# Kernel tuning notes

Hardware: AMD Instinct MI355X
Metric: run time of the kernel (lower is better)

The kernel has to match this reference:

```python
import jax, jax.numpy as jnp
import numpy as np

B, T, C = 128, 512, 1024  # batch, time (fixed by `line` buffer), channels


def fft_convolve(a, b):
    """Linear convolution via zero-padded FFT, sliced to a's length.
    a: (1, C, T) kernel, b: (B, C, T) signal. Returns (B, C, T)."""
    n = a.shape[-1]
    a_pad = jnp.pad(a, ((0, 0), (0, 0), (0, n)))
    b_pad = jnp.pad(b, ((0, 0), (0, 0), (0, n)))
    spec = jnp.fft.rfft(a_pad, axis=-1) * jnp.fft.rfft(b_pad, axis=-1)
    return jnp.fft.irfft(spec, n=2 * n, axis=-1)[..., :n]


def setup_inputs() -> dict:
    key = jax.random.key(0)
    k1, k2, k3, k4, k5 = jax.random.split(key, 5)
    bound = 1.0 / np.sqrt(C)  # nn.Linear default init range
    x = jax.random.normal(k1, (B, T, C), dtype=jnp.float32)
    W_proj = jax.random.uniform(k2, (C, C), jnp.float32, -bound, bound)
    W_values = jax.random.uniform(k3, (C, C), jnp.float32, -bound, bound)
    gain = jax.random.uniform(k4, (1, 1, C), jnp.float32, 0.01, 1.0)
    pow_ = jax.random.uniform(k5, (1, C, 1), jnp.float32, -6.0, 6.0)
    line = jnp.linspace(1.0, 0.0, T, dtype=jnp.float32)[None, None, :]  # (1,1,T)
    return {"x": x, "W_proj": W_proj, "W_values": W_values,
            "gain": gain, "pow_": pow_, "line": line}


def reference(x, W_proj, W_values, gain, pow_, line):
    # proj and values (bias-free Linears)
    h = jnp.einsum('btc,dc->btd', x, W_proj)          # (B,T,C)
    v = jnp.einsum('btc,dc->btd', h, W_values)        # (B,T,C)
    # learned power-law kernel, one decay per channel: (1,C,T)
    z = line ** (2.0 + jax.nn.sigmoid(pow_) * 100.0)
    # FFT long convolution along time
    y = fft_convolve(z, jnp.transpose(v, (0, 2, 1)))  # (B,C,T)
    y = jnp.transpose(y, (0, 2, 1))                    # (B,T,C)
    return jax.nn.relu(y * gain)
```

## Files before the change

### kernel.cpp

```cpp
#include <hip/hip_runtime.h>
#include <hip/hip_bf16.h>

#define B_ 128
#define T_ 512
#define C_ 1024

typedef __attribute__((ext_vector_type(8))) short short8;
typedef __attribute__((ext_vector_type(4))) float f32x4;

__device__ __forceinline__ unsigned short f2bf(float f){
  unsigned u; __builtin_memcpy(&u, &f, 4);
  u += 0x7FFFu + ((u >> 16) & 1u);
  return (unsigned short)(u >> 16);
}

typedef __attribute__((address_space(3))) unsigned lds_u32_t;
typedef __attribute__((address_space(1))) unsigned glb_u32_t;
__device__ __forceinline__ void gload16(const void* g, void* l){
  __builtin_amdgcn_global_load_lds((const glb_u32_t*)g, (lds_u32_t*)l, 16, 0, 0);
}

__global__ void cast_f32_bf16(const float* __restrict__ in, unsigned short* __restrict__ out, long n){
  long i = (long)blockIdx.x * blockDim.x + threadIdx.x;
  long stride = (long)gridDim.x * blockDim.x;
  for (long j = i * 4; j < n; j += stride * 4){
    float4 v = *(const float4*)(in + j);
    ushort4 o; o.x = f2bf(v.x); o.y = f2bf(v.y); o.z = f2bf(v.z); o.w = f2bf(v.w);
    *(ushort4*)(out + j) = o;
  }
}

__global__ void transpose_cast(const float* __restrict__ in, unsigned short* __restrict__ out){
  __shared__ float tile[32][33];
  int c0 = blockIdx.x * 32, e0 = blockIdx.y * 32;
  int tx = threadIdx.x, ty = threadIdx.y;
  for (int r = 0; r < 32; r += 8)
    tile[ty + r][tx] = in[(size_t)(e0 + ty + r) * C_ + c0 + tx];
  __syncthreads();
  for (int r = 0; r < 32; r += 8)
    out[(size_t)(c0 + ty + r) * C_ + e0 + tx] = f2bf(tile[tx][ty + r]);
}

__global__ __launch_bounds__(256) void gemm_bt_bf16(
    const unsigned short* __restrict__ A,
    const unsigned short* __restrict__ Bt,
    unsigned short* __restrict__ Cc,
    int M, int N, int K)
{
  __shared__ short As[128 * 32];
  __shared__ short Bs[128 * 32];
  const int tid  = threadIdx.x;
  const int lane = tid & 63;
  const int wave = tid >> 6;
  const int wr = wave >> 1, wc = wave & 1;
  const int lr = lane & 15, kg = lane >> 4;
  const int m0 = blockIdx.x * 128;
  const int n0 = blockIdx.y * 128;

  f32x4 acc[4][4];
  #pragma unroll
  for (int mi = 0; mi < 4; mi++)
    #pragma unroll
    for (int ni = 0; ni < 4; ni++)
      acc[mi][ni] = (f32x4){0.f, 0.f, 0.f, 0.f};

  const int r1 = tid >> 2, ch1 = tid & 3;
  char* abase = (char*)As + (tid & ~63) * 16;
  char* bbase = (char*)Bs + (tid & ~63) * 16;

  for (int k0 = 0; k0 < K; k0 += 32){
    __syncthreads();
    gload16(A  + (size_t)(m0 + r1)      * K + k0 + ch1 * 8, abase);
    gload16(A  + (size_t)(m0 + 64 + r1) * K + k0 + ch1 * 8, abase + 4096);
    gload16(Bt + (size_t)(n0 + r1)      * K + k0 + ch1 * 8, bbase);
    gload16(Bt + (size_t)(n0 + 64 + r1) * K + k0 + ch1 * 8, bbase + 4096);
    __syncthreads();

    short8 af[4], bfr[4];
    #pragma unroll
    for (int mi = 0; mi < 4; mi++)
      af[mi] = *(const short8*)&As[(wr * 64 + mi * 16 + lr) * 32 + kg * 8];
    #pragma unroll
    for (int ni = 0; ni < 4; ni++)
      bfr[ni] = *(const short8*)&Bs[(wc * 64 + ni * 16 + lr) * 32 + kg * 8];
    #pragma unroll
    for (int mi = 0; mi < 4; mi++)
      #pragma unroll
      for (int ni = 0; ni < 4; ni++)
        acc[mi][ni] = __builtin_amdgcn_mfma_f32_16x16x32_bf16(af[mi], bfr[ni], acc[mi][ni], 0, 0, 0);
  }

  #pragma unroll
  for (int mi = 0; mi < 4; mi++)
    #pragma unroll
    for (int ni = 0; ni < 4; ni++){
      int n = n0 + wc * 64 + ni * 16 + lr;
      int mb = m0 + wr * 64 + mi * 16 + kg * 4;
      #pragma unroll
      for (int j = 0; j < 4; j++)
        Cc[(size_t)(mb + j) * N + n] = f2bf(acc[mi][ni][j]);
    }
}

#define SWZ(x) ((x) ^ ((((x) >> 7) & 3) << 4))

#define STAGE_A(kt, kh) { \
  int d_ = wv * 1024 + ln * 16; int o_ = SWZ(d_); \
  gload16(Ag + (size_t)(m0 + (o_ >> 6)) * 1024 + (kt) * 64 + (kh) * 32 + ((o_ >> 4) & 3) * 8, \
          ldsc + ((kt) & 1) * 32768 + (kh) * 16384 + wv * 1024); \
  d_ += 8192; o_ = SWZ(d_); \
  gload16(Ag + (size_t)(m0 + (o_ >> 6)) * 1024 + (kt) * 64 + (kh) * 32 + ((o_ >> 4) & 3) * 8, \
          ldsc + ((kt) & 1) * 32768 + (kh) * 16384 + 8192 + wv * 1024); }

#define STAGE_B(kt, kh) { \
  int d_ = wv * 1024 + ln * 16; int o_ = SWZ(d_); \
  gload16(Bg + (size_t)(n0 + (o_ >> 6)) * 1024 + (kt) * 64 + (kh) * 32 + ((o_ >> 4) & 3) * 8, \
          ldsc + 65536 + ((kt) & 1) * 32768 + (kh) * 16384 + wv * 1024); \
  d_ += 8192; o_ = SWZ(d_); \
  gload16(Bg + (size_t)(n0 + (o_ >> 6)) * 1024 + (kt) * 64 + (kh) * 32 + ((o_ >> 4) & 3) * 8, \
          ldsc + 65536 + ((kt) & 1) * 32768 + (kh) * 16384 + 8192 + wv * 1024); }

__global__ __launch_bounds__(512, 2) void gemm256_vt(
    const unsigned short* __restrict__ Ag,
    const unsigned short* __restrict__ Bg,
    unsigned short* __restrict__ vt)
{
  extern __shared__ char ldsc[];
  typedef __attribute__((address_space(3))) char lds_char;
  lds_char* lds3 = (lds_char*)ldsc;
  const int tid = threadIdx.x;
  const int ln  = tid & 63;
  const int wv  = tid >> 6;
  const int wr  = wv >> 2;
  const int wc  = wv & 3;
  const int lr  = ln & 15, kg = ln >> 4;
  const int m0  = blockIdx.y * 256;
  const int n0  = blockIdx.x * 256;

  f32x4 acc[8][4];
  #pragma unroll
  for (int mi = 0; mi < 8; mi++)
    #pragma unroll
    for (int ni = 0; ni < 4; ni++)
      acc[mi][ni] = (f32x4){0.f, 0.f, 0.f, 0.f};

  STAGE_A(0, 0); STAGE_A(0, 1); STAGE_B(0, 0); STAGE_B(0, 1);

  short8 af[2][8], bf2[2][4];

  #pragma unroll 1
  for (int t = 0; t < 16; ++t){
    const int S = t & 1;
    if (t < 15){
      STAGE_A(t + 1, 0); STAGE_A(t + 1, 1); STAGE_B(t + 1, 0); STAGE_B(t + 1, 1);
      __builtin_amdgcn_sched_barrier(0);
      asm volatile("s_waitcnt vmcnt(8)");
      __builtin_amdgcn_sched_barrier(0);
    } else {
      __builtin_amdgcn_sched_barrier(0);
      asm volatile("s_waitcnt vmcnt(0)");
      __builtin_amdgcn_sched_barrier(0);
    }
    __builtin_amdgcn_s_barrier();
    __builtin_amdgcn_sched_barrier(0);

    #pragma unroll
    for (int kk = 0; kk < 2; ++kk){
      #pragma unroll
      for (int mi = 0; mi < 8; mi++){
        int off = S * 32768 + kk * 16384 + (wr * 128 + mi * 16 + lr) * 64 + kg * 16;
        unsigned a_ = (unsigned)(size_t)(lds3 + SWZ(off));
        asm volatile("ds_read_b128 %0, %1" : "=v"(af[kk][mi]) : "v"(a_));
      }
      #pragma unroll
      for (int ni = 0; ni < 4; ni++){
        int off = 65536 + S * 32768 + kk * 16384 + (wc * 64 + ni * 16 + lr) * 64 + kg * 16;
        unsigned a_ = (unsigned)(size_t)(lds3 + SWZ(off));
        asm volatile("ds_read_b128 %0, %1" : "=v"(bf2[kk][ni]) : "v"(a_));
      }
    }

    asm volatile("s_waitcnt lgkmcnt(12)");
    __builtin_amdgcn_sched_barrier(0);
    __builtin_amdgcn_s_setprio(1);
    #pragma unroll
    for (int mi = 0; mi < 8; mi++)
      #pragma unroll
      for (int ni = 0; ni < 4; ni++)
        acc[mi][ni] = __builtin_amdgcn_mfma_f32_16x16x32_bf16(af[0][mi], bf2[0][ni], acc[mi][ni], 0, 0, 0);
    __builtin_amdgcn_s_setprio(0);

    asm volatile("s_waitcnt lgkmcnt(0)");
    __builtin_amdgcn_sched_barrier(0);
    __builtin_amdgcn_s_setprio(1);
    #pragma unroll
    for (int mi = 0; mi < 8; mi++)
      #pragma unroll
      for (int ni = 0; ni < 4; ni++)
        acc[mi][ni] = __builtin_amdgcn_mfma_f32_16x16x32_bf16(af[1][mi], bf2[1][ni], acc[mi][ni], 0, 0, 0);
    __builtin_amdgcn_s_setprio(0);
    __builtin_amdgcn_sched_barrier(0);
    __builtin_amdgcn_s_barrier();
  }

  #pragma unroll
  for (int mi = 0; mi < 8; mi++)
    #pragma unroll
    for (int ni = 0; ni < 4; ni++){
      int n  = n0 + wc * 64 + ni * 16 + lr;
      int mb = m0 + wr * 128 + mi * 16 + kg * 4;
      int bb = mb >> 9, t = mb & 511;
      ushort4 o;
      o.x = f2bf(acc[mi][ni][0]); o.y = f2bf(acc[mi][ni][1]);
      o.z = f2bf(acc[mi][ni][2]); o.w = f2bf(acc[mi][ni][3]);
      *(ushort4*)&vt[((size_t)n * B_ + bb) * T_ + t] = o;
    }
}

__global__ void band_prep(const float* __restrict__ pw, const float* __restrict__ line,
                          unsigned short* __restrict__ band){
  const int c = blockIdx.x, d32 = blockIdx.y;
  const float p = pw[c];
  const float e = 2.0f + 100.0f / (1.0f + expf(-p));
  const int tid = threadIdx.x;
  for (int idx = tid; idx < 1280; idx += 256){
    int i = idx / 40, j = idx - i * 40;
    int k = d32 * 32 + i - j;
    float z = 0.f;
    if (j < 32 && k >= 0 && k < T_){
      float lv = line[k];
      z = (lv > 0.f) ? expf(e * logf(lv)) : 0.f;
    }
    band[((size_t)c * 16 + d32) * 1280 + idx] = f2bf(z);
  }
}

__global__ __launch_bounds__(256) void conv_mfma(
    const unsigned short* __restrict__ vt,
    const unsigned short* __restrict__ band,
    const float* __restrict__ gain,
    unsigned short* __restrict__ Ybf)
{
  __shared__ short Bs[128 * 32];
  __shared__ short Ab[16 * 1280];
  const int c   = blockIdx.x;
  const int t0  = blockIdx.y << 7;
  const int tid = threadIdx.x, lane = tid & 63, wave = tid >> 6;
  const int wr = wave >> 1, wc = wave & 1, lr = lane & 15, kg = lane >> 4;
  const int K  = t0 + 128;
  const int nb = (t0 >> 5) + 4;

  {
    const unsigned short* src = band + (size_t)c * (16 * 1280);
    const int nch = nb * 160;
    for (int q0 = 0; q0 < nch; q0 += 256){
      int q = q0 + tid;
      char* dst = (char*)Ab + q0 * 16 + wave * 1024;
      if (q < nch) gload16(src + (size_t)q * 8, dst);
    }
  }

  f32x4 acc[4][4];
  #pragma unroll
  for (int mi = 0; mi < 4; mi++)
    #pragma unroll
    for (int ni = 0; ni < 4; ni++)
      acc[mi][ni] = (f32x4){0.f, 0.f, 0.f, 0.f};

  const int r1 = tid >> 2, ch1 = tid & 3;
  char* bbase = (char*)Bs + (tid & ~63) * 16;
  const size_t vbase = (size_t)c * B_ * T_;

  for (int k0 = 0; k0 < K; k0 += 32){
    __syncthreads();
    gload16(vt + vbase + (size_t)r1 * T_        + k0 + ch1 * 8, bbase);
    gload16(vt + vbase + (size_t)(64 + r1) * T_ + k0 + ch1 * 8, bbase + 4096);
    __syncthreads();

    short8 bfr[4];
    #pragma unroll
    for (int ni = 0; ni < 4; ni++)
      bfr[ni] = *(const short8*)&Bs[(wc * 64 + ni * 16 + lr) * 32 + kg * 8];

    const int dbase = ((t0 - k0) >> 5) + wr * 2;
    #pragma unroll
    for (int mi = 0; mi < 4; mi++){
      const int d32 = dbase + (mi >> 1);
      if (d32 >= 0){
        const int i = ((mi & 1) << 4) + lr;
        short8 af = *(const short8*)&Ab[d32 * 1280 + i * 40 + kg * 8];
        #pragma unroll
        for (int ni = 0; ni < 4; ni++)
          acc[mi][ni] = __builtin_amdgcn_mfma_f32_16x16x32_bf16(af, bfr[ni], acc[mi][ni], 0, 0, 0);
      }
    }
  }

  const float g = gain[c];
  #pragma unroll
  for (int mi = 0; mi < 4; mi++)
    #pragma unroll
    for (int ni = 0; ni < 4; ni++){
      int t = t0 + wr * 64 + mi * 16 + kg * 4;
      int b = wc * 64 + ni * 16 + lr;
      ushort4 o;
      o.x = f2bf(fmaxf(acc[mi][ni][0] * g, 0.f));
      o.y = f2bf(fmaxf(acc[mi][ni][1] * g, 0.f));
      o.z = f2bf(fmaxf(acc[mi][ni][2] * g, 0.f));
      o.w = f2bf(fmaxf(acc[mi][ni][3] * g, 0.f));
      *(ushort4*)&Ybf[((size_t)c * B_ + b) * T_ + t] = o;
    }
}

__global__ __launch_bounds__(256) void final_out(const unsigned short* __restrict__ Ybf,
                                                 float* __restrict__ out){
  __shared__ unsigned short tile[64][72];
  const int c0 = blockIdx.x * 64;
  const int t0 = blockIdx.y * 64;
  const int b  = blockIdx.z;
  const int tid = threadIdx.x;
  const int cr = tid >> 4;
  const int t4 = (tid & 15) * 4;
  for (int q = 0; q < 64; q += 16){
    ushort4 u = *(const ushort4*)&Ybf[((size_t)(c0 + cr + q) * B_ + b) * T_ + t0 + t4];
    *(ushort4*)&tile[cr + q][t4] = u;
  }
  __syncthreads();
  const int tr = tid >> 4;
  const int c4 = (tid & 15) * 4;
  for (int q = 0; q < 64; q += 16){
    int t = tr + q;
    float4 o;
    o.x = __uint_as_float((unsigned)tile[c4 + 0][t] << 16);
    o.y = __uint_as_float((unsigned)tile[c4 + 1][t] << 16);
    o.z = __uint_as_float((unsigned)tile[c4 + 2][t] << 16);
    o.w = __uint_as_float((unsigned)tile[c4 + 3][t] << 16);
    *(float4*)&out[((size_t)b * T_ + t0 + t) * C_ + c0 + c4] = o;
  }
}

extern "C" void kernel_launch(void* const* d_in, const int* in_sizes, int n_in,
                              void* d_out, int out_size, void* d_ws, size_t ws_size,
                              hipStream_t stream)
{
  (void)in_sizes; (void)n_in; (void)out_size; (void)ws_size;
  const float* x    = (const float*)d_in[0];
  const float* Wp   = (const float*)d_in[1];
  const float* Wv   = (const float*)d_in[2];
  const float* gain = (const float*)d_in[3];
  const float* pw   = (const float*)d_in[4];
  const float* line = (const float*)d_in[5];
  float* out = (float*)d_out;

  char* ws = (char*)d_ws;
  unsigned short* Ybf   = (unsigned short*)ws;
  unsigned short* WpT   = (unsigned short*)(ws + 134217728);
  unsigned short* Wv_bf = (unsigned short*)(ws + 134217728 + 2097152);
  unsigned short* W_f   = (unsigned short*)(ws + 134217728 + 2 * 2097152);
  unsigned short* x_bf  = (unsigned short*)d_out;
  unsigned short* vt    = (unsigned short*)d_out + 67108864;
  unsigned short* bandp = (unsigned short*)d_out;

  cast_f32_bf16<<<256, 256, 0, stream>>>(Wv, Wv_bf, (long)C_ * C_);
  transpose_cast<<<dim3(32, 32), dim3(32, 8), 0, stream>>>(Wp, WpT);
  gemm_bt_bf16<<<dim3(8, 8), 256, 0, stream>>>(Wv_bf, WpT, W_f, C_, C_, C_);
  cast_f32_bf16<<<2048, 256, 0, stream>>>(x, x_bf, (long)B_ * T_ * C_);
  gemm256_vt<<<dim3(4, 256), 512, 131072, stream>>>(x_bf, W_f, vt);
  band_prep<<<dim3(1024, 16), 256, 0, stream>>>(pw, line, bandp);
  conv_mfma<<<dim3(1024, 4), 256, 0, stream>>>(vt, bandp, gain, Ybf);
  final_out<<<dim3(16, 8, 128), 256, 0, stream>>>(Ybf, out);
}
```

Measured before the change: 510.4 us.

## Replace 256x256 GEMM tile with 128x128 tiles and XCD-aware block mapping

The main x·W_f GEMM moves from 256x256 tiles with 8 waves and 128KB of LDS to 128x128 tiles with 4 waves, 32KB of LDS and a K step of 32. The grid becomes 1-D, with a mapping that keeps consecutive M tiles on the same XCD so the B operand and nearby A rows are reused in that XCD's L2. Smaller tiles give more blocks and occupancy, but lower arithmetic intensity per LDS load and twice as many barriers per K.

```diff
diff --git a/kernel.cpp b/kernel.cpp
--- a/kernel.cpp
+++ b/kernel.cpp
@@ -16,6 +16,7 @@
 
 typedef __attribute__((address_space(3))) unsigned lds_u32_t;
 typedef __attribute__((address_space(1))) unsigned glb_u32_t;
+typedef __attribute__((address_space(3))) char lds_char;
 __device__ __forceinline__ void gload16(const void* g, void* l){
   __builtin_amdgcn_global_load_lds((const glb_u32_t*)g, (lds_u32_t*)l, 16, 0, 0);
 }
@@ -104,57 +105,53 @@
 
 #define SWZ(x) ((x) ^ ((((x) >> 7) & 3) << 4))
 
-#define STAGE_A(kt, kh) { \
+#define STAGE128(src, base, kt, ldsoff) { \
   int d_ = wv * 1024 + ln * 16; int o_ = SWZ(d_); \
-  gload16(Ag + (size_t)(m0 + (o_ >> 6)) * 1024 + (kt) * 64 + (kh) * 32 + ((o_ >> 4) & 3) * 8, \
-          ldsc + ((kt) & 1) * 32768 + (kh) * 16384 + wv * 1024); \
-  d_ += 8192; o_ = SWZ(d_); \
-  gload16(Ag + (size_t)(m0 + (o_ >> 6)) * 1024 + (kt) * 64 + (kh) * 32 + ((o_ >> 4) & 3) * 8, \
-          ldsc + ((kt) & 1) * 32768 + (kh) * 16384 + 8192 + wv * 1024); }
-
-#define STAGE_B(kt, kh) { \
-  int d_ = wv * 1024 + ln * 16; int o_ = SWZ(d_); \
-  gload16(Bg + (size_t)(n0 + (o_ >> 6)) * 1024 + (kt) * 64 + (kh) * 32 + ((o_ >> 4) & 3) * 8, \
-          ldsc + 65536 + ((kt) & 1) * 32768 + (kh) * 16384 + wv * 1024); \
-  d_ += 8192; o_ = SWZ(d_); \
-  gload16(Bg + (size_t)(n0 + (o_ >> 6)) * 1024 + (kt) * 64 + (kh) * 32 + ((o_ >> 4) & 3) * 8, \
-          ldsc + 65536 + ((kt) & 1) * 32768 + (kh) * 16384 + 8192 + wv * 1024); }
-
-__global__ __launch_bounds__(512, 2) void gemm256_vt(
+  gload16(src + (size_t)(base + (o_ >> 6)) * 1024 + (kt) * 32 + ((o_ >> 4) & 3) * 8, \
+          ldsc + (ldsoff) + wv * 1024); \
+  d_ += 4096; o_ = SWZ(d_); \
+  gload16(src + (size_t)(base + (o_ >> 6)) * 1024 + (kt) * 32 + ((o_ >> 4) & 3) * 8, \
+          ldsc + (ldsoff) + 4096 + wv * 1024); }
+
+__global__ __launch_bounds__(256, 4) void gemm128_vt(
     const unsigned short* __restrict__ Ag,
     const unsigned short* __restrict__ Bg,
     unsigned short* __restrict__ vt)
 {
   extern __shared__ char ldsc[];
-  typedef __attribute__((address_space(3))) char lds_char;
   lds_char* lds3 = (lds_char*)ldsc;
   const int tid = threadIdx.x;
   const int ln  = tid & 63;
   const int wv  = tid >> 6;
-  const int wr  = wv >> 2;
-  const int wc  = wv & 3;
+  const int wr  = wv >> 1;
+  const int wc  = wv & 1;
   const int lr  = ln & 15, kg = ln >> 4;
-  const int m0  = blockIdx.y * 256;
-  const int n0  = blockIdx.x * 256;
-
-  f32x4 acc[8][4];
-  #pragma unroll
-  for (int mi = 0; mi < 8; mi++)
+  const int id  = blockIdx.x;
+  const int xcd = id & 7;
+  const int j   = id >> 3;
+  const int n0  = (j & 7) * 128;
+  const int m0  = (xcd * 64 + (j >> 3)) * 128;
+
+  f32x4 acc[4][4];
+  #pragma unroll
+  for (int mi = 0; mi < 4; mi++)
     #pragma unroll
     for (int ni = 0; ni < 4; ni++)
       acc[mi][ni] = (f32x4){0.f, 0.f, 0.f, 0.f};
 
-  STAGE_A(0, 0); STAGE_A(0, 1); STAGE_B(0, 0); STAGE_B(0, 1);
-
-  short8 af[2][8], bf2[2][4];
+  STAGE128(Ag, m0, 0, 0);
+  STAGE128(Bg, n0, 0, 8192);
+
+  short8 a[4], b[4];
 
   #pragma unroll 1
-  for (int t = 0; t < 16; ++t){
+  for (int t = 0; t < 32; ++t){
     const int S = t & 1;
-    if (t < 15){
-      STAGE_A(t + 1, 0); STAGE_A(t + 1, 1); STAGE_B(t + 1, 0); STAGE_B(t + 1, 1);
+    if (t < 31){
+      STAGE128(Ag, m0, t + 1, (S ^ 1) * 16384);
+      STAGE128(Bg, n0, t + 1, (S ^ 1) * 16384 + 8192);
       __builtin_amdgcn_sched_barrier(0);
-      asm volatile("s_waitcnt vmcnt(8)");
+      asm volatile("s_waitcnt vmcnt(4)");
       __builtin_amdgcn_sched_barrier(0);
     } else {
       __builtin_amdgcn_sched_barrier(0);
@@ -165,50 +162,37 @@
     __builtin_amdgcn_sched_barrier(0);
 
     #pragma unroll
-    for (int kk = 0; kk < 2; ++kk){
-      #pragma unroll
-      for (int mi = 0; mi < 8; mi++){
-        int off = S * 32768 + kk * 16384 + (wr * 128 + mi * 16 + lr) * 64 + kg * 16;
-        unsigned a_ = (unsigned)(size_t)(lds3 + SWZ(off));
-        asm volatile("ds_read_b128 %0, %1" : "=v"(af[kk][mi]) : "v"(a_));
-      }
-      #pragma unroll
-      for (int ni = 0; ni < 4; ni++){
-        int off = 65536 + S * 32768 + kk * 16384 + (wc * 64 + ni * 16 + lr) * 64 + kg * 16;
-        unsigned a_ = (unsigned)(size_t)(lds3 + SWZ(off));
-        asm volatile("ds_read_b128 %0, %1" : "=v"(bf2[kk][ni]) : "v"(a_));
-      }
-    }
-
-    asm volatile("s_waitcnt lgkmcnt(12)");
-    __builtin_amdgcn_sched_barrier(0);
-    __builtin_amdgcn_s_setprio(1);
-    #pragma unroll
-    for (int mi = 0; mi < 8; mi++)
-      #pragma unroll
-      for (int ni = 0; ni < 4; ni++)
-        acc[mi][ni] = __builtin_amdgcn_mfma_f32_16x16x32_bf16(af[0][mi], bf2[0][ni], acc[mi][ni], 0, 0, 0);
-    __builtin_amdgcn_s_setprio(0);
+    for (int mi = 0; mi < 4; mi++){
+      int off = S * 16384 + (wr * 64 + mi * 16 + lr) * 64 + kg * 16;
+      unsigned a_ = (unsigned)(size_t)(lds3 + SWZ(off));
+      asm volatile("ds_read_b128 %0, %1" : "=v"(a[mi]) : "v"(a_));
+    }
+    #pragma unroll
+    for (int ni = 0; ni < 4; ni++){
+      int off = S * 16384 + 8192 + (wc * 64 + ni * 16 + lr) * 64 + kg * 16;
+      unsigned a_ = (unsigned)(size_t)(lds3 + SWZ(off));
+      asm volatile("ds_read_b128 %0, %1" : "=v"(b[ni]) : "v"(a_));
+    }
 
     asm volatile("s_waitcnt lgkmcnt(0)");
     __builtin_amdgcn_sched_barrier(0);
     __builtin_amdgcn_s_setprio(1);
     #pragma unroll
-    for (int mi = 0; mi < 8; mi++)
+    for (int mi = 0; mi < 4; mi++)
       #pragma unroll
       for (int ni = 0; ni < 4; ni++)
-        acc[mi][ni] = __builtin_amdgcn_mfma_f32_16x16x32_bf16(af[1][mi], bf2[1][ni], acc[mi][ni], 0, 0, 0);
+        acc[mi][ni] = __builtin_amdgcn_mfma_f32_16x16x32_bf16(a[mi], b[ni], acc[mi][ni], 0, 0, 0);
     __builtin_amdgcn_s_setprio(0);
     __builtin_amdgcn_sched_barrier(0);
     __builtin_amdgcn_s_barrier();
   }
 
   #pragma unroll
-  for (int mi = 0; mi < 8; mi++)
+  for (int mi = 0; mi < 4; mi++)
     #pragma unroll
     for (int ni = 0; ni < 4; ni++){
       int n  = n0 + wc * 64 + ni * 16 + lr;
-      int mb = m0 + wr * 128 + mi * 16 + kg * 4;
+      int mb = m0 + wr * 64 + mi * 16 + kg * 4;
       int bb = mb >> 9, t = mb & 511;
       ushort4 o;
       o.x = f2bf(acc[mi][ni][0]); o.y = f2bf(acc[mi][ni][1]);
@@ -365,7 +349,7 @@
   transpose_cast<<<dim3(32, 32), dim3(32, 8), 0, stream>>>(Wp, WpT);
   gemm_bt_bf16<<<dim3(8, 8), 256, 0, stream>>>(Wv_bf, WpT, W_f, C_, C_, C_);
   cast_f32_bf16<<<2048, 256, 0, stream>>>(x, x_bf, (long)B_ * T_ * C_);
-  gemm256_vt<<<dim3(4, 256), 512, 131072, stream>>>(x_bf, W_f, vt);
+  gemm128_vt<<<4096, 256, 32768, stream>>>(x_bf, W_f, vt);
   band_prep<<<dim3(1024, 16), 256, 0, stream>>>(pw, line, bandp);
   conv_mfma<<<dim3(1024, 4), 256, 0, stream>>>(vt, bandp, gain, Ybf);
   final_out<<<dim3(16, 8, 128), 256, 0, stream>>>(Ybf, out);
```

Result: slower. 537.2 us (+5.2%).

## Remap GEMM and conv block indices per XCD and simplify band prep

Applied to the files above, without the earlier changes.

The large GEMM and the convolution kernel now launch as 1D grids and remap block IDs. Consecutive blocks on the same XCD (id&7) then work on adjacent tiles or channels, which is meant to improve L2 reuse of shared operands across MI355X's chiplets. The band_prep kernel now computes each of the 63 distinct power-law values once into shared memory and scatters them into the banded matrix. This replaces 1280 exp/log evaluations per block. The remap assumes round-robin dispatch of blocks across 8 XCDs.

```diff
diff --git a/kernel.cpp b/kernel.cpp
--- a/kernel.cpp
+++ b/kernel.cpp
@@ -16,6 +16,7 @@
 
 typedef __attribute__((address_space(3))) unsigned lds_u32_t;
 typedef __attribute__((address_space(1))) unsigned glb_u32_t;
+typedef __attribute__((address_space(3))) char lds_char;
 __device__ __forceinline__ void gload16(const void* g, void* l){
   __builtin_amdgcn_global_load_lds((const glb_u32_t*)g, (lds_u32_t*)l, 16, 0, 0);
 }
@@ -126,7 +127,6 @@
     unsigned short* __restrict__ vt)
 {
   extern __shared__ char ldsc[];
-  typedef __attribute__((address_space(3))) char lds_char;
   lds_char* lds3 = (lds_char*)ldsc;
   const int tid = threadIdx.x;
   const int ln  = tid & 63;
@@ -134,8 +134,10 @@
   const int wr  = wv >> 2;
   const int wc  = wv & 3;
   const int lr  = ln & 15, kg = ln >> 4;
-  const int m0  = blockIdx.y * 256;
-  const int n0  = blockIdx.x * 256;
+  const int id  = blockIdx.x;
+  const int jj  = (id & 7) * 128 + (id >> 3);
+  const int n0  = (jj & 3) * 256;
+  const int m0  = (jj >> 2) * 256;
 
   f32x4 acc[8][4];
   #pragma unroll
@@ -217,21 +219,35 @@
     }
 }
 
-__global__ void band_prep(const float* __restrict__ pw, const float* __restrict__ line,
-                          unsigned short* __restrict__ band){
+__global__ __launch_bounds__(256) void band_prep2(const float* __restrict__ pw,
+                                                  const float* __restrict__ line,
+                                                  unsigned short* __restrict__ band){
+  __shared__ unsigned short zrow[64];
   const int c = blockIdx.x, d32 = blockIdx.y;
-  const float p = pw[c];
-  const float e = 2.0f + 100.0f / (1.0f + expf(-p));
   const int tid = threadIdx.x;
-  for (int idx = tid; idx < 1280; idx += 256){
-    int i = idx / 40, j = idx - i * 40;
-    int k = d32 * 32 + i - j;
+  if (tid < 63){
+    int k = d32 * 32 - 31 + tid;
     float z = 0.f;
-    if (j < 32 && k >= 0 && k < T_){
+    if (k >= 0 && k < T_){
+      float p = pw[c];
+      float e = 2.0f + 100.0f / (1.0f + expf(-p));
       float lv = line[k];
       z = (lv > 0.f) ? expf(e * logf(lv)) : 0.f;
     }
-    band[((size_t)c * 16 + d32) * 1280 + idx] = f2bf(z);
+    zrow[tid] = f2bf(z);
+  }
+  __syncthreads();
+  const size_t base = ((size_t)c * 16 + d32) * 1280;
+  #pragma unroll
+  for (int q = 0; q < 5; q++){
+    int idx = tid + q * 256;
+    int i = idx / 40, j = idx - i * 40;
+    unsigned short v = 0;
+    if (j < 32){
+      int qq = i - j + 31;
+      v = zrow[qq];
+    }
+    band[base + idx] = v;
   }
 }
 
@@ -243,8 +259,11 @@
 {
   __shared__ short Bs[128 * 32];
   __shared__ short Ab[16 * 1280];
-  const int c   = blockIdx.x;
-  const int t0  = blockIdx.y << 7;
+  const int id  = blockIdx.x;
+  const int xcd = id & 7;
+  const int jj  = id >> 3;
+  const int c   = xcd + ((jj >> 2) << 3);
+  const int t0  = (jj & 3) << 7;
   const int tid = threadIdx.x, lane = tid & 63, wave = tid >> 6;
   const int wr = wave >> 1, wc = wave & 1, lr = lane & 15, kg = lane >> 4;
   const int K  = t0 + 128;
@@ -365,8 +384,8 @@
   transpose_cast<<<dim3(32, 32), dim3(32, 8), 0, stream>>>(Wp, WpT);
   gemm_bt_bf16<<<dim3(8, 8), 256, 0, stream>>>(Wv_bf, WpT, W_f, C_, C_, C_);
   cast_f32_bf16<<<2048, 256, 0, stream>>>(x, x_bf, (long)B_ * T_ * C_);
-  gemm256_vt<<<dim3(4, 256), 512, 131072, stream>>>(x_bf, W_f, vt);
-  band_prep<<<dim3(1024, 16), 256, 0, stream>>>(pw, line, bandp);
-  conv_mfma<<<dim3(1024, 4), 256, 0, stream>>>(vt, bandp, gain, Ybf);
+  gemm256_vt<<<1024, 512, 131072, stream>>>(x_bf, W_f, vt);
+  band_prep2<<<dim3(1024, 16), 256, 0, stream>>>(pw, line, bandp);
+  conv_mfma<<<4096, 256, 0, stream>>>(vt, bandp, gain, Ybf);
   final_out<<<dim3(16, 8, 128), 256, 0, stream>>>(Ybf, out);
 }
```

Measured after the change: 522.2 us. 2.3% more time.
